# Kernel tuning notes

Hardware: AMD Instinct MI355X
Metric: run time of the kernel (lower is better)

## Reference

```python
import jax, jax.numpy as jnp
import numpy as np

B_GRAPHS = 32
EMB = 512
ESM = 1280
HEADS = 8
HEAD_DIM = EMB // HEADS


def _segments():
    lengths = 256 + 8 * np.arange(B_GRAPHS)          # 256..504, N = 12160
    batch_ids = np.repeat(np.arange(B_GRAPHS), lengths).astype(np.int32)
    pos = np.concatenate([np.arange(l) for l in lengths]).astype(np.int32)
    return batch_ids, pos, int(lengths.max()), int(lengths.sum())


def setup_inputs() -> dict:
    key = jax.random.key(0)
    ks = jax.random.split(key, 10)
    batch_ids, pos, pad_len, n = _segments()
    s = 0.02
    return {
        "esm_embedding": jax.random.normal(ks[0], (n, ESM), jnp.float32),
        "h": jax.random.normal(ks[1], (n, EMB), jnp.float32),
        "W_esm": jax.random.normal(ks[2], (EMB, ESM), jnp.float32) * s,
        "b_esm": jnp.zeros((EMB,), jnp.float32),
        "Wq": jax.random.normal(ks[3], (EMB, EMB), jnp.float32) * s,
        "bq": jnp.zeros((EMB,), jnp.float32),
        "Wk": jax.random.normal(ks[4], (EMB, EMB), jnp.float32) * s,
        "bk": jnp.zeros((EMB,), jnp.float32),
        "Wv": jax.random.normal(ks[5], (EMB, EMB), jnp.float32) * s,
        "bv": jnp.zeros((EMB,), jnp.float32),
        "Wo": jax.random.normal(ks[6], (EMB, EMB), jnp.float32) * s,
        "bo": jnp.zeros((EMB,), jnp.float32),
        "gamma": jnp.ones((EMB,), jnp.float32),
        "beta": jnp.zeros((EMB,), jnp.float32),
        "batch_ids": jnp.asarray(batch_ids),
        "pos": jnp.asarray(pos),
        "pad_len": pad_len,
        "num_graphs": B_GRAPHS,
    }


def _layer_norm(x, gamma, beta, eps=1e-5):
    mu = jnp.mean(x, axis=-1, keepdims=True)
    var = jnp.var(x, axis=-1, keepdims=True)
    return (x - mu) * jax.lax.rsqrt(var + eps) * gamma + beta


def reference(esm_embedding, h, W_esm, b_esm, Wq, bq, Wk, bk, Wv, bv, Wo, bo,
              gamma, beta, batch_ids, pos, pad_len, num_graphs):
    B, P, D, H, hd = num_graphs, pad_len, EMB, HEADS, HEAD_DIM
    residual = h
    # to_dense_batch: scatter nodes into [B, P, *] padded tensors + key mask
    h_dense = jnp.zeros((B, P, D), h.dtype).at[batch_ids, pos].set(h)
    h_mask = jnp.zeros((B, P), bool).at[batch_ids, pos].set(True)
    h_esm = esm_embedding @ W_esm.T + b_esm                      # [N, D]
    esm_dense = jnp.zeros((B, P, D), h.dtype).at[batch_ids, pos].set(h_esm)

    q = (h_dense @ Wq.T + bq).reshape(B, P, H, hd)
    k = (esm_dense @ Wk.T + bk).reshape(B, P, H, hd)
    v = (esm_dense @ Wv.T + bv).reshape(B, P, H, hd)

    scores = jnp.einsum("bqhd,bkhd->bhqk", q, k) / jnp.sqrt(jnp.float32(hd))
    scores = jnp.where(h_mask[:, None, None, :], scores, -jnp.inf)
    attn = jax.nn.softmax(scores, axis=-1)                        # [B,H,P,P]
    out = jnp.einsum("bhqk,bkhd->bqhd", attn, v).reshape(B, P, D)
    out = out @ Wo.T + bo
    out = out[batch_ids, pos]                                     # unpad -> [N, D]
    return _layer_norm(out + residual, gamma, beta)
```

## Files before the change

### kernel.cpp

```cpp
#include <hip/hip_runtime.h>

#define NTOT 12160
#define EMBD 512
#define ESMD 1280
#define NHEAD 8
#define HD 64
#define NG 32

typedef __attribute__((ext_vector_type(8))) short short8v;
typedef __attribute__((ext_vector_type(4))) short short4v;
typedef __attribute__((ext_vector_type(4))) float floatx4;

__device__ inline short f2bf(float f) {
  union { float f; unsigned u; } v; v.f = f;
  unsigned r = v.u + 0x7fffu + ((v.u >> 16) & 1u);
  return (short)(r >> 16);
}

__device__ inline void gload_lds16(const void* g, void* l) {
  __builtin_amdgcn_global_load_lds((const __attribute__((address_space(1))) void*)g,
                                   (__attribute__((address_space(3))) void*)l, 16, 0, 0);
}

__global__ __launch_bounds__(256) void cvt_kernel(
    const float* __restrict__ esm, const float* __restrict__ h,
    const float* __restrict__ Wesm, const float* __restrict__ Wq,
    const float* __restrict__ Wk, const float* __restrict__ Wv,
    const float* __restrict__ Wo,
    short* __restrict__ esm_b, short* __restrict__ h_b, short* __restrict__ Wesm_b,
    short* __restrict__ Wq_b, short* __restrict__ Wk_b, short* __restrict__ Wv_b,
    short* __restrict__ Wo_b)
{
  int idx = blockIdx.x * 256 + threadIdx.x;
  const float* src; short* dst; int off;
  if      (idx < 3891200) { src = esm;  dst = esm_b;  off = idx; }
  else if (idx < 5447680) { src = h;    dst = h_b;    off = idx - 3891200; }
  else if (idx < 5611520) { src = Wesm; dst = Wesm_b; off = idx - 5447680; }
  else if (idx < 5677056) { src = Wq;   dst = Wq_b;   off = idx - 5611520; }
  else if (idx < 5742592) { src = Wk;   dst = Wk_b;   off = idx - 5677056; }
  else if (idx < 5808128) { src = Wv;   dst = Wv_b;   off = idx - 5742592; }
  else                    { src = Wo;   dst = Wo_b;   off = idx - 5808128; }
  const float4 v = *(const float4*)&src[(size_t)off * 4];
  short4v s; s[0] = f2bf(v.x); s[1] = f2bf(v.y); s[2] = f2bf(v.z); s[3] = f2bf(v.w);
  *(short4v*)&dst[(size_t)off * 4] = s;
}

__device__ inline void gemm_core(const short* __restrict__ A, const short* __restrict__ W,
                                 int K, int row0, int col0,
                                 short* As, short* Bs, floatx4 acc[4][4])
{
  const int tid = threadIdx.x;
  const int lane = tid & 63, wave = tid >> 6;
  const int l15 = lane & 15, quad = lane >> 4;
  const int wm = (wave >> 1) * 64, wn = (wave & 1) * 64;
  const int lrow = lane >> 3;
  const int lcol = (lane & 7) * 8;

  for (int k0 = 0; k0 < K; k0 += 64) {
    if (k0) __syncthreads();
    for (int p = 0; p < 4; p++) {
      int seg = wave * 4 + p;
      gload_lds16(&A[(size_t)(row0 + seg * 8 + lrow) * K + k0 + lcol], &As[seg * 512]);
    }
    for (int p = 0; p < 4; p++) {
      int seg = wave * 4 + p;
      gload_lds16(&W[(size_t)(col0 + seg * 8 + lrow) * K + k0 + lcol], &Bs[seg * 512]);
    }
    __syncthreads();
    for (int ks = 0; ks < 64; ks += 32) {
      short8v a[4], b[4];
      for (int mt = 0; mt < 4; mt++)
        a[mt] = *(const short8v*)&As[(wm + mt * 16 + l15) * 64 + ks + quad * 8];
      for (int nt = 0; nt < 4; nt++)
        b[nt] = *(const short8v*)&Bs[(wn + nt * 16 + l15) * 64 + ks + quad * 8];
      for (int mt = 0; mt < 4; mt++)
        for (int nt = 0; nt < 4; nt++)
          acc[mt][nt] = __builtin_amdgcn_mfma_f32_16x16x32_bf16(a[mt], b[nt], acc[mt][nt], 0, 0, 0);
    }
  }
}

__device__ inline void epi_bf16(floatx4 acc[4][4], const float* bias, short* C,
                                int row0, int col0, int wm, int wn, int l15, int quad)
{
  for (int nt = 0; nt < 4; nt++) {
    int col = col0 + wn + nt * 16 + l15;
    float bv = bias[col];
    for (int mt = 0; mt < 4; mt++) {
      int rowb = row0 + wm + mt * 16 + quad * 4;
      for (int r = 0; r < 4; r++)
        C[(size_t)(rowb + r) * EMBD + col] = f2bf(acc[mt][nt][r] + bv);
    }
  }
}

__global__ __launch_bounds__(256) void esm_gemm(
    const short* __restrict__ A, const short* __restrict__ W,
    const float* __restrict__ bias, short* __restrict__ C)
{
  __shared__ short As[128 * 64];
  __shared__ short Bs[128 * 64];
  floatx4 acc[4][4];
  for (int i = 0; i < 4; i++) for (int j = 0; j < 4; j++)
    for (int r = 0; r < 4; r++) acc[i][j][r] = 0.f;
  const int row0 = blockIdx.y * 128, col0 = blockIdx.x * 128;
  gemm_core(A, W, ESMD, row0, col0, As, Bs, acc);
  const int lane = threadIdx.x & 63, wave = threadIdx.x >> 6;
  epi_bf16(acc, bias, C, row0, col0, (wave >> 1) * 64, (wave & 1) * 64, lane & 15, lane >> 4);
}

__global__ __launch_bounds__(256) void qkv_gemm(
    const short* __restrict__ hb, const short* __restrict__ hesm,
    const short* __restrict__ Wq, const short* __restrict__ Wk, const short* __restrict__ Wv,
    const float* __restrict__ bq, const float* __restrict__ bk, const float* __restrict__ bv,
    short* __restrict__ qb, short* __restrict__ kb, short* __restrict__ vt)
{
  __shared__ short As[128 * 64];
  __shared__ short Bs[128 * 64];
  const int which = blockIdx.x >> 2;
  const int row0 = blockIdx.y * 128, col0 = (blockIdx.x & 3) * 128;
  const short* A = (which == 0) ? hb : hesm;
  const short* W = (which == 0) ? Wq : (which == 1 ? Wk : Wv);
  const float* bias = (which == 0) ? bq : (which == 1 ? bk : bv);
  floatx4 acc[4][4];
  for (int i = 0; i < 4; i++) for (int j = 0; j < 4; j++)
    for (int r = 0; r < 4; r++) acc[i][j][r] = 0.f;
  gemm_core(A, W, EMBD, row0, col0, As, Bs, acc);
  const int lane = threadIdx.x & 63, wave = threadIdx.x >> 6;
  const int l15 = lane & 15, quad = lane >> 4;
  const int wm = (wave >> 1) * 64, wn = (wave & 1) * 64;
  if (which < 2) {
    epi_bf16(acc, bias, which ? kb : qb, row0, col0, wm, wn, l15, quad);
  } else {
    for (int nt = 0; nt < 4; nt++) {
      int col = col0 + wn + nt * 16 + l15;
      float bv2 = bias[col];
      for (int mt = 0; mt < 4; mt++) {
        int rowb = row0 + wm + mt * 16 + quad * 4;
        short4v sv;
        for (int r = 0; r < 4; r++) sv[r] = f2bf(acc[mt][nt][r] + bv2);
        *(short4v*)&vt[(size_t)col * NTOT + rowb] = sv;
      }
    }
  }
}

__global__ __launch_bounds__(256) void o_gemm(
    const short* __restrict__ A, const short* __restrict__ W,
    const float* __restrict__ bias, float* __restrict__ C)
{
  __shared__ short As[128 * 64];
  __shared__ short Bs[128 * 64];
  floatx4 acc[4][4];
  for (int i = 0; i < 4; i++) for (int j = 0; j < 4; j++)
    for (int r = 0; r < 4; r++) acc[i][j][r] = 0.f;
  const int row0 = blockIdx.y * 128, col0 = blockIdx.x * 128;
  gemm_core(A, W, EMBD, row0, col0, As, Bs, acc);
  const int lane = threadIdx.x & 63, wave = threadIdx.x >> 6;
  const int l15 = lane & 15, quad = lane >> 4;
  const int wm = (wave >> 1) * 64, wn = (wave & 1) * 64;
  for (int nt = 0; nt < 4; nt++) {
    int col = col0 + wn + nt * 16 + l15;
    float bv = bias[col];
    for (int mt = 0; mt < 4; mt++) {
      int rowb = row0 + wm + mt * 16 + quad * 4;
      for (int r = 0; r < 4; r++)
        C[(size_t)(rowb + r) * EMBD + col] = acc[mt][nt][r] + bv;
    }
  }
}

template<bool MASK>
__device__ inline void attn_chunk(
    int kc, int L, int start, size_t hoff,
    const short* __restrict__ kb, const short* __restrict__ vt,
    short* Ps, const short8v& aq0, const short8v& aq1,
    floatx4 oacc[4], float rowsum[4], int l15, int quad)
{
  floatx4 s[4];
  for (int sub = 0; sub < 4; sub++) {
    int kr = kc + sub * 16 + l15;
    if (MASK) kr = min(kr, L - 1);
    const short* kp = &kb[(size_t)(start + kr) * EMBD + hoff + quad * 8];
    short8v b0 = *(const short8v*)kp;
    short8v b1 = *(const short8v*)(kp + 32);
    floatx4 c; for (int r = 0; r < 4; r++) c[r] = 0.f;
    c = __builtin_amdgcn_mfma_f32_16x16x32_bf16(aq0, b0, c, 0, 0, 0);
    c = __builtin_amdgcn_mfma_f32_16x16x32_bf16(aq1, b1, c, 0, 0, 0);
    s[sub] = c;
  }
  for (int sub = 0; sub < 4; sub++)
    for (int r = 0; r < 4; r++) {
      float p = __expf(s[sub][r] * 0.125f);
      if (MASK && (kc + sub * 16 + l15 >= L)) p = 0.f;
      rowsum[r] += p;
      Ps[(quad * 4 + r) * 72 + sub * 16 + l15] = f2bf(p);
    }
  for (int half = 0; half < 2; half++) {
    short8v pA = *(const short8v*)&Ps[l15 * 72 + half * 32 + quad * 8];
    int kb2 = kc + half * 32 + quad * 8;
    if (MASK) kb2 = min(kb2, L - 8);
    for (int dt = 0; dt < 4; dt++) {
      const short8v bvv = *(const short8v*)&vt[(size_t)(hoff + dt * 16 + l15) * NTOT + start + kb2];
      oacc[dt] = __builtin_amdgcn_mfma_f32_16x16x32_bf16(pA, bvv, oacc[dt], 0, 0, 0);
    }
  }
}

__global__ __launch_bounds__(512) void attn_kernel(
    const short* __restrict__ qb, const short* __restrict__ kb,
    const short* __restrict__ vt, short* __restrict__ ao)
{
  __shared__ short Ps_all[8][16 * 72];
  const int x = blockIdx.x & 7, j = blockIdx.x >> 3;
  int g = -1, qt = 0, acc = 0;
  for (int i = 0; i < 4; i++) {
    int gg = x + 8 * i;
    int t = 16 + ((gg + 1) >> 1);
    if (j < acc + t) { g = gg; qt = j - acc; break; }
    acc += t;
  }
  if (g < 0) return;
  const int L = 256 + 8 * g;
  const int start = 256 * g + 4 * g * (g - 1);
  const int h = threadIdx.x >> 6;
  const int lane = threadIdx.x & 63;
  const int l15 = lane & 15, quad = lane >> 4;
  const size_t hoff = (size_t)h * HD;
  short* Ps = Ps_all[h];

  int qrow = qt * 16 + l15;
  if (qrow > L - 1) qrow = L - 1;
  const size_t qoff = (size_t)(start + qrow) * EMBD + hoff + quad * 8;
  const short8v aq0 = *(const short8v*)&qb[qoff];
  const short8v aq1 = *(const short8v*)&qb[qoff + 32];

  float rowsum[4];
  floatx4 oacc[4];
  for (int r = 0; r < 4; r++) rowsum[r] = 0.f;
  for (int dt = 0; dt < 4; dt++)
    for (int r = 0; r < 4; r++) oacc[dt][r] = 0.f;

  const int Lfull = L & ~63;
  for (int kc = 0; kc < Lfull; kc += 64)
    attn_chunk<false>(kc, L, start, hoff, kb, vt, Ps, aq0, aq1, oacc, rowsum, l15, quad);
  if (Lfull < L)
    attn_chunk<true>(Lfull, L, start, hoff, kb, vt, Ps, aq0, aq1, oacc, rowsum, l15, quad);

  float inv[4];
  for (int r = 0; r < 4; r++) {
    float red = rowsum[r];
    red += __shfl_xor(red, 1); red += __shfl_xor(red, 2);
    red += __shfl_xor(red, 4); red += __shfl_xor(red, 8);
    inv[r] = 1.f / red;
  }
  for (int dt = 0; dt < 4; dt++)
    for (int r = 0; r < 4; r++) {
      int rl = qt * 16 + quad * 4 + r;
      if (rl < L)
        ao[(size_t)(start + rl) * EMBD + hoff + dt * 16 + l15] = f2bf(oacc[dt][r] * inv[r]);
    }
}

__global__ __launch_bounds__(64) void ln_kernel(
    float* __restrict__ y, const float* __restrict__ hres,
    const float* __restrict__ gamma, const float* __restrict__ beta)
{
  const int row = blockIdx.x;
  const int lane = threadIdx.x;
  const size_t base = (size_t)row * EMBD + lane * 8;
  const float4 a0 = *(const float4*)&y[base];
  const float4 a1 = *(const float4*)&y[base + 4];
  const float4 b0 = *(const float4*)&hres[base];
  const float4 b1 = *(const float4*)&hres[base + 4];
  float x[8] = { a0.x + b0.x, a0.y + b0.y, a0.z + b0.z, a0.w + b0.w,
                 a1.x + b1.x, a1.y + b1.y, a1.z + b1.z, a1.w + b1.w };
  float s = 0.f, s2 = 0.f;
  for (int i = 0; i < 8; i++) { s += x[i]; s2 += x[i] * x[i]; }
  for (int off = 1; off < 64; off <<= 1) { s += __shfl_xor(s, off); s2 += __shfl_xor(s2, off); }
  const float mu = s * (1.f / 512.f);
  const float var = s2 * (1.f / 512.f) - mu * mu;
  const float rstd = rsqrtf(var + 1e-5f);
  const float4 g0 = *(const float4*)&gamma[lane * 8];
  const float4 g1 = *(const float4*)&gamma[lane * 8 + 4];
  const float4 e0 = *(const float4*)&beta[lane * 8];
  const float4 e1 = *(const float4*)&beta[lane * 8 + 4];
  const float gg[8] = { g0.x, g0.y, g0.z, g0.w, g1.x, g1.y, g1.z, g1.w };
  const float ee[8] = { e0.x, e0.y, e0.z, e0.w, e1.x, e1.y, e1.z, e1.w };
  float o[8];
  for (int i = 0; i < 8; i++) o[i] = (x[i] - mu) * rstd * gg[i] + ee[i];
  *(float4*)&y[base]     = make_float4(o[0], o[1], o[2], o[3]);
  *(float4*)&y[base + 4] = make_float4(o[4], o[5], o[6], o[7]);
}

extern "C" void kernel_launch(void* const* d_in, const int* in_sizes, int n_in,
                              void* d_out, int out_size, void* d_ws, size_t ws_size,
                              hipStream_t stream)
{
  (void)in_sizes; (void)n_in; (void)out_size; (void)ws_size;
  const float* esm   = (const float*)d_in[0];
  const float* h     = (const float*)d_in[1];
  const float* Wesm  = (const float*)d_in[2];
  const float* besm  = (const float*)d_in[3];
  const float* Wq    = (const float*)d_in[4];
  const float* bq    = (const float*)d_in[5];
  const float* Wk    = (const float*)d_in[6];
  const float* bk    = (const float*)d_in[7];
  const float* Wv    = (const float*)d_in[8];
  const float* bv    = (const float*)d_in[9];
  const float* Wo    = (const float*)d_in[10];
  const float* bo    = (const float*)d_in[11];
  const float* gamma = (const float*)d_in[12];
  const float* beta  = (const float*)d_in[13];

  char* ws = (char*)d_ws;
  short* esm_b  = (short*)ws;
  short* h_b    = (short*)(ws + 31129600);
  short* Wesm_b = (short*)(ws + 43581440);
  short* Wq_b   = (short*)(ws + 44892160);
  short* Wk_b   = (short*)(ws + 45416448);
  short* Wv_b   = (short*)(ws + 45940736);
  short* Wo_b   = (short*)(ws + 46465024);
  short* hesm   = (short*)(ws + 46989312);
  short* qb     = (short*)ws;
  short* kb     = (short*)(ws + 12451840);
  short* ao     = h_b;
  short* vt     = (short*)d_out;
  float* y      = (float*)d_out;

  cvt_kernel<<<dim3(22944), dim3(256), 0, stream>>>(
      esm, h, Wesm, Wq, Wk, Wv, Wo, esm_b, h_b, Wesm_b, Wq_b, Wk_b, Wv_b, Wo_b);
  esm_gemm<<<dim3(4, 95), dim3(256), 0, stream>>>(esm_b, Wesm_b, besm, hesm);
  qkv_gemm<<<dim3(12, 95), dim3(256), 0, stream>>>(
      h_b, hesm, Wq_b, Wk_b, Wv_b, bq, bk, bv, qb, kb, vt);
  attn_kernel<<<dim3(832), dim3(512), 0, stream>>>(qb, kb, vt, ao);
  o_gemm<<<dim3(4, 95), dim3(256), 0, stream>>>(ao, Wo_b, bo, y);
  ln_kernel<<<dim3(NTOT), dim3(64), 0, stream>>>(y, h, gamma, beta);
}
```

Baseline: 352.5 us.

## Fold ESM projection into K/V weights and tile K/V layouts for attention

Precomputes Wk·W_esm and Wv·W_esm, plus the fused biases, so K and V are computed directly from the ESM embedding. This removes the separate esm_gemm and the hesm intermediate, but the K and V GEMMs now use K=1280 instead of 512. The h conversion pass is dropped: the Q GEMM reads fp32 h and converts it to bf16 while staging into LDS. K and V are written in per-head, per-16-row-tile packed layouts, so attention loads are contiguous instead of strided. This adds extra rounding from the fused bf16 weights and more GEMM FLOPs overall.

```diff
diff --git a/kernel.cpp b/kernel.cpp
--- a/kernel.cpp
+++ b/kernel.cpp
@@ -6,6 +6,7 @@
 #define NHEAD 8
 #define HD 64
 #define NG 32
+#define NTILE 768
 
 typedef __attribute__((ext_vector_type(8))) short short8v;
 typedef __attribute__((ext_vector_type(4))) short short4v;
@@ -22,30 +23,69 @@
                                    (__attribute__((address_space(3))) void*)l, 16, 0, 0);
 }
 
+__device__ inline int node_graph(int n) {
+  int g = (int)((sqrtf(3969.f + (float)n) - 63.f) * 0.5f);
+  if (4 * (g + 1) * (g + 64) <= n) g++;
+  else if (4 * g * (g + 63) > n) g--;
+  return g;
+}
+
 __global__ __launch_bounds__(256) void cvt_kernel(
-    const float* __restrict__ esm, const float* __restrict__ h,
-    const float* __restrict__ Wesm, const float* __restrict__ Wq,
+    const float* __restrict__ esm, const float* __restrict__ Wq,
     const float* __restrict__ Wk, const float* __restrict__ Wv,
     const float* __restrict__ Wo,
-    short* __restrict__ esm_b, short* __restrict__ h_b, short* __restrict__ Wesm_b,
-    short* __restrict__ Wq_b, short* __restrict__ Wk_b, short* __restrict__ Wv_b,
-    short* __restrict__ Wo_b)
+    short* __restrict__ esm_b, short* __restrict__ Wq_b,
+    short* __restrict__ Wk_b, short* __restrict__ Wv_b, short* __restrict__ Wo_b)
 {
   int idx = blockIdx.x * 256 + threadIdx.x;
   const float* src; short* dst; int off;
-  if      (idx < 3891200) { src = esm;  dst = esm_b;  off = idx; }
-  else if (idx < 5447680) { src = h;    dst = h_b;    off = idx - 3891200; }
-  else if (idx < 5611520) { src = Wesm; dst = Wesm_b; off = idx - 5447680; }
-  else if (idx < 5677056) { src = Wq;   dst = Wq_b;   off = idx - 5611520; }
-  else if (idx < 5742592) { src = Wk;   dst = Wk_b;   off = idx - 5677056; }
-  else if (idx < 5808128) { src = Wv;   dst = Wv_b;   off = idx - 5742592; }
-  else                    { src = Wo;   dst = Wo_b;   off = idx - 5808128; }
+  if      (idx < 3891200) { src = esm; dst = esm_b; off = idx; }
+  else if (idx < 3956736) { src = Wq;  dst = Wq_b;  off = idx - 3891200; }
+  else if (idx < 4022272) { src = Wk;  dst = Wk_b;  off = idx - 3956736; }
+  else if (idx < 4087808) { src = Wv;  dst = Wv_b;  off = idx - 4022272; }
+  else                    { src = Wo;  dst = Wo_b;  off = idx - 4087808; }
   const float4 v = *(const float4*)&src[(size_t)off * 4];
   short4v s; s[0] = f2bf(v.x); s[1] = f2bf(v.y); s[2] = f2bf(v.z); s[3] = f2bf(v.w);
   *(short4v*)&dst[(size_t)off * 4] = s;
 }
 
-__device__ inline void gemm_core(const short* __restrict__ A, const short* __restrict__ W,
+__global__ __launch_bounds__(256) void wtrans_kernel(
+    const float* __restrict__ W, short* __restrict__ WT)
+{
+  __shared__ short t[32][33];
+  const int c0 = blockIdx.x * 32;
+  const int r0 = blockIdx.y * 32;
+  const int tr = threadIdx.x >> 5, tc = threadIdx.x & 31;
+  for (int i = 0; i < 4; i++)
+    t[i * 8 + tr][tc] = f2bf(W[(size_t)(r0 + i * 8 + tr) * 1280 + c0 + tc]);
+  __syncthreads();
+  for (int i = 0; i < 4; i++)
+    WT[(size_t)(c0 + i * 8 + tr) * 512 + r0 + tc] = t[tc][i * 8 + tr];
+}
+
+__global__ __launch_bounds__(256) void bfuse_kernel(
+    const float* __restrict__ Wk, const float* __restrict__ Wv,
+    const float* __restrict__ besm, const float* __restrict__ bk,
+    const float* __restrict__ bv, float* __restrict__ bkp, float* __restrict__ bvp)
+{
+  int wgid = blockIdx.x * 4 + (threadIdx.x >> 6);
+  int lane = threadIdx.x & 63;
+  const float* W  = (wgid < 512) ? Wk : Wv;
+  const float* ba = (wgid < 512) ? bk : bv;
+  float* o        = (wgid < 512) ? bkp : bvp;
+  int row = wgid & 511;
+  const float4 w0 = *(const float4*)&W[(size_t)row * 512 + lane * 8];
+  const float4 w1 = *(const float4*)&W[(size_t)row * 512 + lane * 8 + 4];
+  const float4 b0 = *(const float4*)&besm[lane * 8];
+  const float4 b1 = *(const float4*)&besm[lane * 8 + 4];
+  float s = w0.x * b0.x + w0.y * b0.y + w0.z * b0.z + w0.w * b0.w
+          + w1.x * b1.x + w1.y * b1.y + w1.z * b1.z + w1.w * b1.w;
+  for (int off = 1; off < 64; off <<= 1) s += __shfl_xor(s, off);
+  if (lane == 0) o[row] = s + ba[row];
+}
+
+template<int AF32>
+__device__ inline void gemm_core(const void* __restrict__ Ap, const short* __restrict__ W,
                                  int K, int row0, int col0,
                                  short* As, short* Bs, floatx4 acc[4][4])
 {
@@ -58,9 +98,21 @@
 
   for (int k0 = 0; k0 < K; k0 += 64) {
     if (k0) __syncthreads();
-    for (int p = 0; p < 4; p++) {
-      int seg = wave * 4 + p;
-      gload_lds16(&A[(size_t)(row0 + seg * 8 + lrow) * K + k0 + lcol], &As[seg * 512]);
+    if (AF32) {
+      const float* A = (const float*)Ap;
+      for (int p = 0; p < 8; p++) {
+        int idx = p * 256 + tid;
+        int r = idx >> 4, c4 = idx & 15;
+        const float4 v = *(const float4*)&A[(size_t)(row0 + r) * K + k0 + c4 * 4];
+        short4v sv; sv[0] = f2bf(v.x); sv[1] = f2bf(v.y); sv[2] = f2bf(v.z); sv[3] = f2bf(v.w);
+        *(short4v*)&As[r * 64 + c4 * 4] = sv;
+      }
+    } else {
+      const short* A = (const short*)Ap;
+      for (int p = 0; p < 4; p++) {
+        int seg = wave * 4 + p;
+        gload_lds16(&A[(size_t)(row0 + seg * 8 + lrow) * K + k0 + lcol], &As[seg * 512]);
+      }
     }
     for (int p = 0; p < 4; p++) {
       int seg = wave * 4 + p;
@@ -94,9 +146,191 @@
   }
 }
 
-__global__ __launch_bounds__(256) void esm_gemm(
+__global__ __launch_bounds__(256) void wfuse_gemm(
+    const short* __restrict__ Wk_b, const short* __restrict__ Wv_b,
+    const short* __restrict__ WT, short* __restrict__ Wkp, short* __restrict__ Wvp)
+{
+  __shared__ short As[128 * 64];
+  __shared__ short Bs[128 * 64];
+  const int wh = blockIdx.x >= 10;
+  const int col0 = (blockIdx.x - (wh ? 10 : 0)) * 128;
+  const int row0 = blockIdx.y * 128;
+  floatx4 acc[4][4];
+  for (int i = 0; i < 4; i++) for (int j = 0; j < 4; j++)
+    for (int r = 0; r < 4; r++) acc[i][j][r] = 0.f;
+  gemm_core<0>(wh ? Wv_b : Wk_b, WT, 512, row0, col0, As, Bs, acc);
+  short* O = wh ? Wvp : Wkp;
+  const int lane = threadIdx.x & 63, wave = threadIdx.x >> 6;
+  const int l15 = lane & 15, quad = lane >> 4;
+  const int wm = (wave >> 1) * 64, wn = (wave & 1) * 64;
+  for (int nt = 0; nt < 4; nt++) {
+    int col = col0 + wn + nt * 16 + l15;
+    for (int mt = 0; mt < 4; mt++) {
+      int rowb = row0 + wm + mt * 16 + quad * 4;
+      for (int r = 0; r < 4; r++)
+        O[(size_t)(rowb + r) * ESMD + col] = f2bf(acc[mt][nt][r]);
+    }
+  }
+}
+
+__global__ __launch_bounds__(256) void qkv_gemm(
+    const float* __restrict__ hf, const short* __restrict__ esm_b,
+    const short* __restrict__ Wq_b, const short* __restrict__ Wkp, const short* __restrict__ Wvp,
+    const float* __restrict__ bq, const float* __restrict__ bkp, const float* __restrict__ bvp,
+    short* __restrict__ qb, short* __restrict__ kp, short* __restrict__ vp)
+{
+  __shared__ short As[128 * 64];
+  __shared__ short Bs[128 * 64];
+  const int which = blockIdx.x >> 2;
+  const int row0 = blockIdx.y * 128, col0 = (blockIdx.x & 3) * 128;
+  floatx4 acc[4][4];
+  for (int i = 0; i < 4; i++) for (int j = 0; j < 4; j++)
+    for (int r = 0; r < 4; r++) acc[i][j][r] = 0.f;
+  if (which == 0) gemm_core<1>(hf,    Wq_b, 512,  row0, col0, As, Bs, acc);
+  else if (which == 1) gemm_core<0>(esm_b, Wkp, 1280, row0, col0, As, Bs, acc);
+  else gemm_core<0>(esm_b, Wvp, 1280, row0, col0, As, Bs, acc);
+
+  const int lane = threadIdx.x & 63, wave = threadIdx.x >> 6;
+  const int l15 = lane & 15, quad = lane >> 4;
+  const int wm = (wave >> 1) * 64, wn = (wave & 1) * 64;
+
+  if (which == 0) {
+    epi_bf16(acc, bq, qb, row0, col0, wm, wn, l15, quad);
+  } else if (which == 1) {
+    for (int mt = 0; mt < 4; mt++) {
+      int rowb = row0 + wm + mt * 16 + quad * 4;
+      int g = node_graph(rowb);
+      int loc = rowb - 4 * g * (g + 63);
+      int ptile = 16 * g + (g * g) / 4 + (loc >> 4);
+      int l15k = loc & 15;
+      for (int nt = 0; nt < 4; nt++) {
+        int col = col0 + wn + nt * 16 + l15;
+        float bv = bkp[col];
+        int hh = col >> 6, dh = col & 63;
+        int hfh = dh >> 5, qk = (dh & 31) >> 3, jk = dh & 7;
+        size_t base = ((size_t)(hh * NTILE + ptile) * 2 + hfh) * 512
+                      + (size_t)l15k * 32 + qk * 8 + jk;
+        for (int r = 0; r < 4; r++)
+          kp[base + (size_t)r * 32] = f2bf(acc[mt][nt][r] + bv);
+      }
+    }
+  } else {
+    for (int mt = 0; mt < 4; mt++) {
+      int rowb = row0 + wm + mt * 16 + quad * 4;
+      int g = node_graph(rowb);
+      int loc = rowb - 4 * g * (g + 63);
+      int ptile = 16 * g + (g * g) / 4 + (loc >> 4);
+      int koff = loc & 15;
+      for (int nt = 0; nt < 4; nt++) {
+        int col = col0 + wn + nt * 16 + l15;
+        float bv = bvp[col];
+        int hh = col >> 6, dh = col & 63;
+        int dt = dh >> 4, l15v = dh & 15;
+        size_t base = ((size_t)(hh * 4 + dt) * NTILE + ptile) * 256
+                      + (size_t)l15v * 16 + koff;
+        short4v sv;
+        for (int r = 0; r < 4; r++) sv[r] = f2bf(acc[mt][nt][r] + bv);
+        *(short4v*)&vp[base] = sv;
+      }
+    }
+  }
+}
+
+template<bool MASK>
+__device__ inline void attn_chunk(
+    int kc, int L, int Tg, int hb, int hdt4,
+    const short* __restrict__ kp, const short* __restrict__ vp,
+    short* Ps, const short8v& aq0, const short8v& aq1,
+    floatx4 oacc[4], float rowsum[4], int l15, int quad)
+{
+  floatx4 s[4];
+  const int t0 = Tg + (kc >> 4);
+  for (int sub = 0; sub < 4; sub++) {
+    const short* kpt = &kp[((size_t)(hb + t0 + sub) * 2) * 512 + l15 * 32 + quad * 8];
+    short8v b0 = *(const short8v*)kpt;
+    short8v b1 = *(const short8v*)(kpt + 512);
+    floatx4 c; for (int r = 0; r < 4; r++) c[r] = 0.f;
+    c = __builtin_amdgcn_mfma_f32_16x16x32_bf16(aq0, b0, c, 0, 0, 0);
+    c = __builtin_amdgcn_mfma_f32_16x16x32_bf16(aq1, b1, c, 0, 0, 0);
+    s[sub] = c;
+  }
+  for (int sub = 0; sub < 4; sub++)
+    for (int r = 0; r < 4; r++) {
+      float p = __expf(s[sub][r] * 0.125f);
+      if (MASK && (kc + sub * 16 + l15 >= L)) p = 0.f;
+      rowsum[r] += p;
+      Ps[(quad * 4 + r) * 72 + sub * 16 + l15] = f2bf(p);
+    }
+  for (int half = 0; half < 2; half++) {
+    short8v pA = *(const short8v*)&Ps[l15 * 72 + half * 32 + quad * 8];
+    for (int dt = 0; dt < 4; dt++) {
+      size_t vbase = ((size_t)(hdt4 + dt) * NTILE + t0 + half * 2 + (quad >> 1)) * 256
+                     + (size_t)l15 * 16 + (quad & 1) * 8;
+      short8v bvv = *(const short8v*)&vp[vbase];
+      oacc[dt] = __builtin_amdgcn_mfma_f32_16x16x32_bf16(pA, bvv, oacc[dt], 0, 0, 0);
+    }
+  }
+}
+
+__global__ __launch_bounds__(512) void attn_kernel(
+    const short* __restrict__ qb, const short* __restrict__ kp,
+    const short* __restrict__ vp, short* __restrict__ ao)
+{
+  __shared__ short Ps_all[8][16 * 72];
+  const int x = blockIdx.x & 7, j = blockIdx.x >> 3;
+  int g = -1, qt = 0, accum = 0;
+  for (int i = 0; i < 4; i++) {
+    int gg = x + 8 * i;
+    int t = 16 + ((gg + 1) >> 1);
+    if (j < accum + t) { g = gg; qt = j - accum; break; }
+    accum += t;
+  }
+  if (g < 0) return;
+  const int L = 256 + 8 * g;
+  const int start = 4 * g * (g + 63);
+  const int Tg = 16 * g + (g * g) / 4;
+  const int h = threadIdx.x >> 6;
+  const int lane = threadIdx.x & 63;
+  const int l15 = lane & 15, quad = lane >> 4;
+  const int hb = h * NTILE, hdt4 = h * 4;
+  short* Ps = Ps_all[h];
+
+  int qrow = qt * 16 + l15;
+  if (qrow > L - 1) qrow = L - 1;
+  const size_t qoff = (size_t)(start + qrow) * EMBD + h * HD + quad * 8;
+  const short8v aq0 = *(const short8v*)&qb[qoff];
+  const short8v aq1 = *(const short8v*)&qb[qoff + 32];
+
+  float rowsum[4];
+  floatx4 oacc[4];
+  for (int r = 0; r < 4; r++) rowsum[r] = 0.f;
+  for (int dt = 0; dt < 4; dt++)
+    for (int r = 0; r < 4; r++) oacc[dt][r] = 0.f;
+
+  const int Lfull = L & ~63;
+  for (int kc = 0; kc < Lfull; kc += 64)
+    attn_chunk<false>(kc, L, Tg, hb, hdt4, kp, vp, Ps, aq0, aq1, oacc, rowsum, l15, quad);
+  if (Lfull < L)
+    attn_chunk<true>(Lfull, L, Tg, hb, hdt4, kp, vp, Ps, aq0, aq1, oacc, rowsum, l15, quad);
+
+  float inv[4];
+  for (int r = 0; r < 4; r++) {
+    float red = rowsum[r];
+    red += __shfl_xor(red, 1); red += __shfl_xor(red, 2);
+    red += __shfl_xor(red, 4); red += __shfl_xor(red, 8);
+    inv[r] = 1.f / red;
+  }
+  for (int dt = 0; dt < 4; dt++)
+    for (int r = 0; r < 4; r++) {
+      int rl = qt * 16 + quad * 4 + r;
+      if (rl < L)
+        ao[(size_t)(start + rl) * EMBD + h * HD + dt * 16 + l15] = f2bf(oacc[dt][r] * inv[r]);
+    }
+}
+
+__global__ __launch_bounds__(256) void o_gemm(
     const short* __restrict__ A, const short* __restrict__ W,
-    const float* __restrict__ bias, short* __restrict__ C)
+    const float* __restrict__ bias, float* __restrict__ C)
 {
   __shared__ short As[128 * 64];
   __shared__ short Bs[128 * 64];
@@ -104,58 +338,7 @@
   for (int i = 0; i < 4; i++) for (int j = 0; j < 4; j++)
     for (int r = 0; r < 4; r++) acc[i][j][r] = 0.f;
   const int row0 = blockIdx.y * 128, col0 = blockIdx.x * 128;
-  gemm_core(A, W, ESMD, row0, col0, As, Bs, acc);
-  const int lane = threadIdx.x & 63, wave = threadIdx.x >> 6;
-  epi_bf16(acc, bias, C, row0, col0, (wave >> 1) * 64, (wave & 1) * 64, lane & 15, lane >> 4);
-}
-
-__global__ __launch_bounds__(256) void qkv_gemm(
-    const short* __restrict__ hb, const short* __restrict__ hesm,
-    const short* __restrict__ Wq, const short* __restrict__ Wk, const short* __restrict__ Wv,
-    const float* __restrict__ bq, const float* __restrict__ bk, const float* __restrict__ bv,
-    short* __restrict__ qb, short* __restrict__ kb, short* __restrict__ vt)
-{
-  __shared__ short As[128 * 64];
-  __shared__ short Bs[128 * 64];
-  const int which = blockIdx.x >> 2;
-  const int row0 = blockIdx.y * 128, col0 = (blockIdx.x & 3) * 128;
-  const short* A = (which == 0) ? hb : hesm;
-  const short* W = (which == 0) ? Wq : (which == 1 ? Wk : Wv);
-  const float* bias = (which == 0) ? bq : (which == 1 ? bk : bv);
-  floatx4 acc[4][4];
-  for (int i = 0; i < 4; i++) for (int j = 0; j < 4; j++)
-    for (int r = 0; r < 4; r++) acc[i][j][r] = 0.f;
-  gemm_core(A, W, EMBD, row0, col0, As, Bs, acc);
-  const int lane = threadIdx.x & 63, wave = threadIdx.x >> 6;
-  const int l15 = lane & 15, quad = lane >> 4;
-  const int wm = (wave >> 1) * 64, wn = (wave & 1) * 64;
-  if (which < 2) {
-    epi_bf16(acc, bias, which ? kb : qb, row0, col0, wm, wn, l15, quad);
-  } else {
-    for (int nt = 0; nt < 4; nt++) {
-      int col = col0 + wn + nt * 16 + l15;
-      float bv2 = bias[col];
-      for (int mt = 0; mt < 4; mt++) {
-        int rowb = row0 + wm + mt * 16 + quad * 4;
-        short4v sv;
-        for (int r = 0; r < 4; r++) sv[r] = f2bf(acc[mt][nt][r] + bv2);
-        *(short4v*)&vt[(size_t)col * NTOT + rowb] = sv;
-      }
-    }
-  }
-}
-
-__global__ __launch_bounds__(256) void o_gemm(
-    const short* __restrict__ A, const short* __restrict__ W,
-    const float* __restrict__ bias, float* __restrict__ C)
-{
-  __shared__ short As[128 * 64];
-  __shared__ short Bs[128 * 64];
-  floatx4 acc[4][4];
-  for (int i = 0; i < 4; i++) for (int j = 0; j < 4; j++)
-    for (int r = 0; r < 4; r++) acc[i][j][r] = 0.f;
-  const int row0 = blockIdx.y * 128, col0 = blockIdx.x * 128;
-  gemm_core(A, W, EMBD, row0, col0, As, Bs, acc);
+  gemm_core<0>(A, W, EMBD, row0, col0, As, Bs, acc);
   const int lane = threadIdx.x & 63, wave = threadIdx.x >> 6;
   const int l15 = lane & 15, quad = lane >> 4;
   const int wm = (wave >> 1) * 64, wn = (wave & 1) * 64;
@@ -168,98 +351,6 @@
         C[(size_t)(rowb + r) * EMBD + col] = acc[mt][nt][r] + bv;
     }
   }
-}
-
-template<bool MASK>
-__device__ inline void attn_chunk(
-    int kc, int L, int start, size_t hoff,
-    const short* __restrict__ kb, const short* __restrict__ vt,
-    short* Ps, const short8v& aq0, const short8v& aq1,
-    floatx4 oacc[4], float rowsum[4], int l15, int quad)
-{
-  floatx4 s[4];
-  for (int sub = 0; sub < 4; sub++) {
-    int kr = kc + sub * 16 + l15;
-    if (MASK) kr = min(kr, L - 1);
-    const short* kp = &kb[(size_t)(start + kr) * EMBD + hoff + quad * 8];
-    short8v b0 = *(const short8v*)kp;
-    short8v b1 = *(const short8v*)(kp + 32);
-    floatx4 c; for (int r = 0; r < 4; r++) c[r] = 0.f;
-    c = __builtin_amdgcn_mfma_f32_16x16x32_bf16(aq0, b0, c, 0, 0, 0);
-    c = __builtin_amdgcn_mfma_f32_16x16x32_bf16(aq1, b1, c, 0, 0, 0);
-    s[sub] = c;
-  }
-  for (int sub = 0; sub < 4; sub++)
-    for (int r = 0; r < 4; r++) {
-      float p = __expf(s[sub][r] * 0.125f);
-      if (MASK && (kc + sub * 16 + l15 >= L)) p = 0.f;
-      rowsum[r] += p;
-      Ps[(quad * 4 + r) * 72 + sub * 16 + l15] = f2bf(p);
-    }
-  for (int half = 0; half < 2; half++) {
-    short8v pA = *(const short8v*)&Ps[l15 * 72 + half * 32 + quad * 8];
-    int kb2 = kc + half * 32 + quad * 8;
-    if (MASK) kb2 = min(kb2, L - 8);
-    for (int dt = 0; dt < 4; dt++) {
-      const short8v bvv = *(const short8v*)&vt[(size_t)(hoff + dt * 16 + l15) * NTOT + start + kb2];
-      oacc[dt] = __builtin_amdgcn_mfma_f32_16x16x32_bf16(pA, bvv, oacc[dt], 0, 0, 0);
-    }
-  }
-}
-
-__global__ __launch_bounds__(512) void attn_kernel(
-    const short* __restrict__ qb, const short* __restrict__ kb,
-    const short* __restrict__ vt, short* __restrict__ ao)
-{
-  __shared__ short Ps_all[8][16 * 72];
-  const int x = blockIdx.x & 7, j = blockIdx.x >> 3;
-  int g = -1, qt = 0, acc = 0;
-  for (int i = 0; i < 4; i++) {
-    int gg = x + 8 * i;
-    int t = 16 + ((gg + 1) >> 1);
-    if (j < acc + t) { g = gg; qt = j - acc; break; }
-    acc += t;
-  }
-  if (g < 0) return;
-  const int L = 256 + 8 * g;
-  const int start = 256 * g + 4 * g * (g - 1);
-  const int h = threadIdx.x >> 6;
-  const int lane = threadIdx.x & 63;
-  const int l15 = lane & 15, quad = lane >> 4;
-  const size_t hoff = (size_t)h * HD;
-  short* Ps = Ps_all[h];
-
-  int qrow = qt * 16 + l15;
-  if (qrow > L - 1) qrow = L - 1;
-  const size_t qoff = (size_t)(start + qrow) * EMBD + hoff + quad * 8;
-  const short8v aq0 = *(const short8v*)&qb[qoff];
-  const short8v aq1 = *(const short8v*)&qb[qoff + 32];
-
-  float rowsum[4];
-  floatx4 oacc[4];
-  for (int r = 0; r < 4; r++) rowsum[r] = 0.f;
-  for (int dt = 0; dt < 4; dt++)
-    for (int r = 0; r < 4; r++) oacc[dt][r] = 0.f;
-
-  const int Lfull = L & ~63;
-  for (int kc = 0; kc < Lfull; kc += 64)
-    attn_chunk<false>(kc, L, start, hoff, kb, vt, Ps, aq0, aq1, oacc, rowsum, l15, quad);
-  if (Lfull < L)
-    attn_chunk<true>(Lfull, L, start, hoff, kb, vt, Ps, aq0, aq1, oacc, rowsum, l15, quad);
-
-  float inv[4];
-  for (int r = 0; r < 4; r++) {
-    float red = rowsum[r];
-    red += __shfl_xor(red, 1); red += __shfl_xor(red, 2);
-    red += __shfl_xor(red, 4); red += __shfl_xor(red, 8);
-    inv[r] = 1.f / red;
-  }
-  for (int dt = 0; dt < 4; dt++)
-    for (int r = 0; r < 4; r++) {
-      int rl = qt * 16 + quad * 4 + r;
-      if (rl < L)
-        ao[(size_t)(start + rl) * EMBD + hoff + dt * 16 + l15] = f2bf(oacc[dt][r] * inv[r]);
-    }
 }
 
 __global__ __launch_bounds__(64) void ln_kernel(
@@ -315,25 +406,29 @@
 
   char* ws = (char*)d_ws;
   short* esm_b  = (short*)ws;
-  short* h_b    = (short*)(ws + 31129600);
-  short* Wesm_b = (short*)(ws + 43581440);
-  short* Wq_b   = (short*)(ws + 44892160);
-  short* Wk_b   = (short*)(ws + 45416448);
-  short* Wv_b   = (short*)(ws + 45940736);
-  short* Wo_b   = (short*)(ws + 46465024);
-  short* hesm   = (short*)(ws + 46989312);
-  short* qb     = (short*)ws;
-  short* kb     = (short*)(ws + 12451840);
-  short* ao     = h_b;
-  short* vt     = (short*)d_out;
+  short* ao     = esm_b;
+  short* kp     = (short*)(ws + 31129600);
+  short* WesmT  = kp;
+  short* vp     = (short*)(ws + 43712512);
+  short* Wq_b   = (short*)(ws + 56295424);
+  short* Wk_b   = (short*)(ws + 56819712);
+  short* Wv_b   = (short*)(ws + 57344000);
+  short* Wo_b   = (short*)(ws + 57868288);
+  short* Wkp    = (short*)(ws + 58392576);
+  short* Wvp    = (short*)(ws + 59703296);
+  float* bkp    = (float*)(ws + 61014016);
+  float* bvp    = (float*)(ws + 61016064);
+  short* qb     = (short*)d_out;
   float* y      = (float*)d_out;
 
-  cvt_kernel<<<dim3(22944), dim3(256), 0, stream>>>(
-      esm, h, Wesm, Wq, Wk, Wv, Wo, esm_b, h_b, Wesm_b, Wq_b, Wk_b, Wv_b, Wo_b);
-  esm_gemm<<<dim3(4, 95), dim3(256), 0, stream>>>(esm_b, Wesm_b, besm, hesm);
+  cvt_kernel<<<dim3(16224), dim3(256), 0, stream>>>(
+      esm, Wq, Wk, Wv, Wo, esm_b, Wq_b, Wk_b, Wv_b, Wo_b);
+  wtrans_kernel<<<dim3(40, 16), dim3(256), 0, stream>>>(Wesm, WesmT);
+  bfuse_kernel<<<dim3(256), dim3(256), 0, stream>>>(Wk, Wv, besm, bk, bv, bkp, bvp);
+  wfuse_gemm<<<dim3(20, 4), dim3(256), 0, stream>>>(Wk_b, Wv_b, WesmT, Wkp, Wvp);
   qkv_gemm<<<dim3(12, 95), dim3(256), 0, stream>>>(
-      h_b, hesm, Wq_b, Wk_b, Wv_b, bq, bk, bv, qb, kb, vt);
-  attn_kernel<<<dim3(832), dim3(512), 0, stream>>>(qb, kb, vt, ao);
+      h, esm_b, Wq_b, Wkp, Wvp, bq, bkp, bvp, qb, kp, vp);
+  attn_kernel<<<dim3(832), dim3(512), 0, stream>>>(qb, kp, vp, ao);
   o_gemm<<<dim3(4, 95), dim3(256), 0, stream>>>(ao, Wo_b, bo, y);
   ln_kernel<<<dim3(NTOT), dim3(64), 0, stream>>>(y, h, gamma, beta);
 }
```

Result: faster. 340.1 us (-3.5%).
